# Optimization experiments

Measured on AMD Instinct MI355X. Metric: run time of the kernel, lower is better.

The kernel has to match this reference:

```python
import jax, jax.numpy as jnp
import numpy as np


def setup_inputs() -> dict:
    key = jax.random.key(0)
    ks = jax.random.split(key, 16)
    B, S, D = 2, 2048, 1024
    H, SH, RH = 16, 1, 3
    hd = D // H
    w = 1.0 / np.sqrt(D)
    return {
        "x": jax.random.normal(ks[0], (B, S, D), jnp.float32),
        "Wq": jax.random.normal(ks[1], (D, D), jnp.float32) * w,
        "bq": jnp.zeros((D,), jnp.float32),
        "Wk": jax.random.normal(ks[2], (D, D), jnp.float32) * w,
        "bk": jnp.zeros((D,), jnp.float32),
        "Wv": jax.random.normal(ks[3], (D, D), jnp.float32) * w,
        "bv": jnp.zeros((D,), jnp.float32),
        "Wproj": jax.random.normal(ks[4], (D, D), jnp.float32) * w,
        "bproj": jnp.zeros((D,), jnp.float32),
        "Wr": jax.random.normal(ks[5], (D, H - SH), jnp.float32) * w,
        "br": jnp.zeros((H - SH,), jnp.float32),
        "Ws": jax.random.normal(ks[6], (D, 2), jnp.float32) * w,
        "bs": jnp.zeros((2,), jnp.float32),
        "temperature": jnp.zeros((H, 1, 1), jnp.float32),
        "query_embedding": jax.random.truncated_normal(ks[7], -2.0, 2.0, (H, 1, hd), jnp.float32) * 0.02,
        "num_heads": H,
        "shared_heads": SH,
        "routed_heads": RH,
    }


def reference(x, Wq, bq, Wk, bk, Wv, bv, Wproj, bproj, Wr, br, Ws, bs,
              temperature, query_embedding, num_heads, shared_heads, routed_heads):
    B, S, D = x.shape
    H = num_heads
    hd = D // H

    def split_heads(t):  # [B,S,D] -> [B,H,S,hd]
        return t.reshape(B, S, H, hd).transpose(0, 2, 1, 3)

    q = split_heads(x @ Wq + bq)
    k = split_heads(x @ Wk + bk)
    v = split_heads(x @ Wv + bv)

    # L2-normalize q along head_dim, add learned query embedding, scale by softplus(temperature)
    q_norm = q * jax.lax.rsqrt(jnp.sum(q * q, axis=-1, keepdims=True) + 1e-12)
    q_scaled = (q_norm + query_embedding[None]) * jax.nn.softplus(temperature)[None]

    attn = jnp.einsum('bhqd,bhkd->bhqk', q_scaled, k) / jnp.sqrt(jnp.float32(hd))
    attn = jax.nn.softmax(attn, axis=-1)
    o = jnp.einsum('bhqk,bhkd->bhqd', attn, v)
    o = o.transpose(0, 2, 1, 3).reshape(B, S, D)  # [B,S,D]

    # Routed-head gating via top-k router
    gates = jax.nn.softmax(o @ Wr + br, axis=-1)          # [B,S,H-SH]
    _, idx = jax.lax.top_k(gates, routed_heads)           # [B,S,RH]
    mask = jax.nn.one_hot(idx, H - shared_heads, dtype=gates.dtype).sum(axis=2)
    routed_gates = gates * mask * jnp.float32(routed_heads)

    # Shared-head gating
    sw = jax.nn.softmax(o @ Ws + bs, axis=-1)             # [B,S,2]
    shared_gates = sw * jnp.float32(shared_heads)
    w0 = sw * 2.0
    shared_gates = w0[..., 0:1] * shared_gates
    routed_gates = w0[..., 1:2] * routed_gates
    masked_gates = jnp.concatenate([shared_gates, routed_gates], axis=-1)

    # einsum('bnh,bnd->bnd') sums over h: scales o by sum of gates
    o = masked_gates.sum(axis=-1, keepdims=True) * o
    return o @ Wproj + bproj
```

## Files before the change

kernel.cpp:

```cpp
#include <hip/hip_runtime.h>
#include <hip/hip_bf16.h>

typedef unsigned short ushort_t;
typedef unsigned int uint_t;

typedef __attribute__((ext_vector_type(8))) short bf8;
typedef __attribute__((ext_vector_type(4))) float f4;
typedef __attribute__((ext_vector_type(16))) float f16v;

__device__ __forceinline__ float bf2f(ushort_t u) {
    unsigned int x = ((unsigned int)u) << 16;
    return __uint_as_float(x);
}
__device__ __forceinline__ ushort_t f2bf(float f) {
    unsigned int x = __float_as_uint(f);
    unsigned int r = x + 0x7fffu + ((x >> 16) & 1u);
    return (ushort_t)(r >> 16);
}
__device__ __forceinline__ uint_t pack2bf(float a, float b) {
    return (uint_t)f2bf(a) | ((uint_t)f2bf(b) << 16);
}

__device__ __forceinline__ void gl2lds16(const ushort_t* g, ushort_t* l) {
    __builtin_amdgcn_global_load_lds(
        (const __attribute__((address_space(1))) void*)g,
        (__attribute__((address_space(3))) void*)l, 16, 0, 0);
}

__global__ __launch_bounds__(256)
void prep(const float* __restrict__ src, ushort_t* __restrict__ dst,
          const float* __restrict__ Wr, const float* __restrict__ Ws,
          ushort_t* __restrict__ Wg)
{
    int bid = blockIdx.x;
    if (bid < 4096) {
        int i = bid * 256 + threadIdx.x;
        float4 v = ((const float4*)src)[i];
        uint2 o;
        o.x = pack2bf(v.x, v.y);
        o.y = pack2bf(v.z, v.w);
        ((uint2*)dst)[i] = o;
    } else {
        int idx = (bid - 4096) * 256 + threadIdx.x;
        int c = idx >> 10, d = idx & 1023;
        float v = 0.f;
        if (c < 15) v = Wr[(size_t)d * 15 + c];
        else if (c < 17) v = Ws[(size_t)d * 2 + (c - 15)];
        Wg[idx] = f2bf(v);
    }
}

__global__ __launch_bounds__(256)
void wtrans(const float* __restrict__ W0, const float* __restrict__ W1,
            const float* __restrict__ W2, const float* __restrict__ W3,
            ushort_t* __restrict__ T0, ushort_t* __restrict__ T1,
            ushort_t* __restrict__ T2, ushort_t* __restrict__ T3)
{
    __shared__ float tile[32][33];
    const float* W; ushort_t* T;
    switch (blockIdx.z) {
        case 0: W = W0; T = T0; break;
        case 1: W = W1; T = T1; break;
        case 2: W = W2; T = T2; break;
        default: W = W3; T = T3; break;
    }
    int k0 = blockIdx.x * 32, n0 = blockIdx.y * 32;
    int t = threadIdx.x;
    int r = t >> 3, c4 = (t & 7) * 4;
    float4 v = *(const float4*)&W[(size_t)(k0 + r) * 1024 + n0 + c4];
    tile[r][c4 + 0] = v.x; tile[r][c4 + 1] = v.y;
    tile[r][c4 + 2] = v.z; tile[r][c4 + 3] = v.w;
    __syncthreads();
    int n = t >> 3, kk = (t & 7) * 4;
    uint2 o;
    o.x = pack2bf(tile[kk][n], tile[kk + 1][n]);
    o.y = pack2bf(tile[kk + 2][n], tile[kk + 3][n]);
    *(uint2*)&T[(size_t)(n0 + n) * 1024 + k0 + kk] = o;
}

__global__ __launch_bounds__(256)
void gemmQKV(const ushort_t* __restrict__ A, const ushort_t* __restrict__ Wt3,
             const float* __restrict__ bq, const float* __restrict__ bk,
             const float* __restrict__ bv,
             ushort_t* __restrict__ Qb, ushort_t* __restrict__ Kw,
             ushort_t* __restrict__ VTw,
             const float* __restrict__ temp, const float* __restrict__ emb)
{
    const int K = 1024;
    __shared__ ushort_t As[128 * 32];
    __shared__ ushort_t Bs[128 * 32];

    int t = threadIdx.x;
    int m0 = blockIdx.x * 128;
    int y = blockIdx.y;
    int region = y >> 3;
    int n0 = (y & 7) * 128;

    int lane = t & 63, w = t >> 6;
    int lm = lane & 15, quad = lane >> 4;
    int wm = (w >> 1) * 64, wn = (w & 1) * 64;

    f4 acc[4][4] = {};

    const ushort_t* pA = &A[(size_t)(m0 + (t >> 2)) * K + (t & 3) * 8];
    const ushort_t* pB = &Wt3[(size_t)(y * 128 + (t >> 2)) * K + (t & 3) * 8];
    ushort_t* lA = &As[t * 8];
    ushort_t* lB = &Bs[t * 8];
    const size_t rstep = (size_t)64 * K;

    for (int k0 = 0; k0 < K; k0 += 32) {
        gl2lds16(pA, lA);
        gl2lds16(pA + rstep, lA + 2048);
        gl2lds16(pB, lB);
        gl2lds16(pB + rstep, lB + 2048);
        pA += 32; pB += 32;
        __syncthreads();

        bf8 af[4], bfr[4];
        #pragma unroll
        for (int mi = 0; mi < 4; mi++)
            af[mi] = *(bf8*)&As[(wm + mi * 16 + lm) * 32 + quad * 8];
        #pragma unroll
        for (int ni = 0; ni < 4; ni++)
            bfr[ni] = *(bf8*)&Bs[(wn + ni * 16 + lm) * 32 + quad * 8];
        if (region == 2) {
            #pragma unroll
            for (int mi = 0; mi < 4; mi++)
            #pragma unroll
            for (int ni = 0; ni < 4; ni++)
                acc[mi][ni] = __builtin_amdgcn_mfma_f32_16x16x32_bf16(af[mi], bfr[ni], acc[mi][ni], 0, 0, 0);
        } else {
            #pragma unroll
            for (int ni = 0; ni < 4; ni++)
            #pragma unroll
            for (int mi = 0; mi < 4; mi++)
                acc[ni][mi] = __builtin_amdgcn_mfma_f32_16x16x32_bf16(bfr[ni], af[mi], acc[ni][mi], 0, 0, 0);
        }
        __syncthreads();
    }

    if (region == 0) {
        int head = (n0 + wn) >> 6;
        float sp = log1pf(__expf(temp[head]));
        f4 bv4[4], ev4[4];
        #pragma unroll
        for (int ni = 0; ni < 4; ni++) {
            bv4[ni] = *(const f4*)&bq[n0 + wn + ni * 16 + quad * 4];
            ev4[ni] = *(const f4*)&emb[head * 64 + ni * 16 + quad * 4];
        }
        #pragma unroll
        for (int mi = 0; mi < 4; mi++) {
            float v[4][4];
            float ss = 0.f;
            #pragma unroll
            for (int ni = 0; ni < 4; ni++)
            #pragma unroll
            for (int i = 0; i < 4; i++) {
                v[ni][i] = acc[ni][mi][i] + bv4[ni][i];
                ss += v[ni][i] * v[ni][i];
            }
            ss += __shfl_xor(ss, 16, 64);
            ss += __shfl_xor(ss, 32, 64);
            float rs = rsqrtf(ss + 1e-12f);
            int tok = m0 + wm + mi * 16 + lm;
            int b = tok >> 11, s = tok & 2047;
            size_t rowb = (((size_t)(b * 16 + head)) * 2048 + s) * 64;
            #pragma unroll
            for (int ni = 0; ni < 4; ni++) {
                uint2 o;
                o.x = pack2bf((v[ni][0] * rs + ev4[ni][0]) * sp * 0.125f,
                              (v[ni][1] * rs + ev4[ni][1]) * sp * 0.125f);
                o.y = pack2bf((v[ni][2] * rs + ev4[ni][2]) * sp * 0.125f,
                              (v[ni][3] * rs + ev4[ni][3]) * sp * 0.125f);
                *(uint2*)&Qb[rowb + ni * 16 + quad * 4] = o;
            }
        }
    } else if (region == 1) {
        int head = (n0 + wn) >> 6;
        f4 bv4[4];
        #pragma unroll
        for (int ni = 0; ni < 4; ni++)
            bv4[ni] = *(const f4*)&bk[n0 + wn + ni * 16 + quad * 4];
        #pragma unroll
        for (int mi = 0; mi < 4; mi++) {
            int tok = m0 + wm + mi * 16 + lm;
            int b = tok >> 11, s = tok & 2047;
            size_t rowb = (((size_t)(b * 16 + head)) * 2048 + s) * 64;
            #pragma unroll
            for (int ni = 0; ni < 4; ni++) {
                uint2 o;
                o.x = pack2bf(acc[ni][mi][0] + bv4[ni][0], acc[ni][mi][1] + bv4[ni][1]);
                o.y = pack2bf(acc[ni][mi][2] + bv4[ni][2], acc[ni][mi][3] + bv4[ni][3]);
                *(uint2*)&Kw[rowb + ni * 16 + quad * 4] = o;
            }
        }
    } else {
        float bvv[4];
        #pragma unroll
        for (int ni = 0; ni < 4; ni++) bvv[ni] = bv[n0 + wn + ni * 16 + lm];
        #pragma unroll
        for (int mi = 0; mi < 4; mi++) {
            int gr0 = m0 + wm + mi * 16 + quad * 4;
            int b = gr0 >> 11, s0 = gr0 & 2047;
            #pragma unroll
            for (int ni = 0; ni < 4; ni++) {
                int gc = n0 + wn + ni * 16 + lm;
                int h = gc >> 6, d = gc & 63;
                uint2 o;
                o.x = pack2bf(acc[mi][ni][0] + bvv[ni], acc[mi][ni][1] + bvv[ni]);
                o.y = pack2bf(acc[mi][ni][2] + bvv[ni], acc[mi][ni][3] + bvv[ni]);
                *(uint2*)&VTw[(((size_t)(b * 16 + h)) * 64 + d) * 2048 + s0] = o;
            }
        }
    }
}

__global__ __launch_bounds__(256)
void gemmP(const ushort_t* __restrict__ A, const ushort_t* __restrict__ Wt,
           const float* __restrict__ bias, const float* __restrict__ G,
           float* __restrict__ out, int M, int N, int K)
{
    __shared__ ushort_t As[128 * 32];
    __shared__ ushort_t Bs[128 * 32];

    int t = threadIdx.x;
    int m0 = blockIdx.x * 128, n0 = blockIdx.y * 128;
    int lane = t & 63, w = t >> 6;
    int lm = lane & 15, quad = lane >> 4;
    int wm = (w >> 1) * 64, wn = (w & 1) * 64;

    f4 acc[4][4] = {};

    const ushort_t* pA = &A[(size_t)(m0 + (t >> 2)) * K + (t & 3) * 8];
    const ushort_t* pB = &Wt[(size_t)(n0 + (t >> 2)) * K + (t & 3) * 8];
    ushort_t* lA = &As[t * 8];
    ushort_t* lB = &Bs[t * 8];
    const size_t rstep = (size_t)64 * K;

    for (int k0 = 0; k0 < K; k0 += 32) {
        gl2lds16(pA, lA);
        gl2lds16(pA + rstep, lA + 2048);
        gl2lds16(pB, lB);
        gl2lds16(pB + rstep, lB + 2048);
        pA += 32; pB += 32;
        __syncthreads();

        bf8 af[4], bfr[4];
        #pragma unroll
        for (int mi = 0; mi < 4; mi++)
            af[mi] = *(bf8*)&As[(wm + mi * 16 + lm) * 32 + quad * 8];
        #pragma unroll
        for (int ni = 0; ni < 4; ni++)
            bfr[ni] = *(bf8*)&Bs[(wn + ni * 16 + lm) * 32 + quad * 8];
        #pragma unroll
        for (int ni = 0; ni < 4; ni++)
        #pragma unroll
        for (int mi = 0; mi < 4; mi++)
            acc[ni][mi] = __builtin_amdgcn_mfma_f32_16x16x32_bf16(bfr[ni], af[mi], acc[ni][mi], 0, 0, 0);
        __syncthreads();
    }

    f4 bv4[4];
    #pragma unroll
    for (int ni = 0; ni < 4; ni++)
        bv4[ni] = *(const f4*)&bias[n0 + wn + ni * 16 + quad * 4];
    #pragma unroll
    for (int mi = 0; mi < 4; mi++) {
        int tok = m0 + wm + mi * 16 + lm;
        float g = G[tok];
        size_t rowb = (size_t)tok * N + n0 + wn;
        #pragma unroll
        for (int ni = 0; ni < 4; ni++) {
            f4 o;
            #pragma unroll
            for (int i = 0; i < 4; i++) o[i] = g * acc[ni][mi][i] + bv4[ni][i];
            *(f4*)&out[rowb + ni * 16 + quad * 4] = o;
        }
    }
}

__global__ __launch_bounds__(256)
void attn(const ushort_t* __restrict__ Q, const ushort_t* __restrict__ K,
          const ushort_t* __restrict__ VT, ushort_t* __restrict__ O)
{
    __shared__ ushort_t Ks[64 * 72];
    __shared__ ushort_t Vt[64 * 72];
    __shared__ ushort_t Ps[4][32 * 72];

    int t = threadIdx.x, lane = t & 63, w = t >> 6;
    int l31 = lane & 31, hi = lane >> 5;
    int bid = blockIdx.x;
    int bh = bid & 31, qt = bid >> 5;
    size_t base = (size_t)bh * 2048 * 64;

    int tok = qt * 128 + w * 32 + l31;
    const ushort_t* qp = &Q[base + (size_t)tok * 64 + hi * 8];
    bf8 qa[4];
    #pragma unroll
    for (int c = 0; c < 4; c++) qa[c] = *(const bf8*)(qp + c * 16);

    float l_part = 0.f;
    f16v o_acc[2] = {};

    int sr = t >> 3, sc = (t & 7) * 8;
    const ushort_t* kg0 = &K[base + (size_t)sr * 64 + sc];
    const ushort_t* vg0 = &VT[base + (size_t)sr * 2048 + sc];

    for (int kb = 0; kb < 2048; kb += 64) {
        __syncthreads();
        {
            uint4 k0 = *(const uint4*)(kg0 + (size_t)kb * 64);
            uint4 k1 = *(const uint4*)(kg0 + (size_t)(kb + 32) * 64);
            uint4 v0 = *(const uint4*)(vg0 + kb);
            uint4 v1 = *(const uint4*)(vg0 + 32 * 2048 + kb);
            *(uint4*)&Ks[sr * 72 + sc] = k0;
            *(uint4*)&Ks[(sr + 32) * 72 + sc] = k1;
            *(uint4*)&Vt[sr * 72 + sc] = v0;
            *(uint4*)&Vt[(sr + 32) * 72 + sc] = v1;
        }
        __syncthreads();

        ushort_t* pw = &Ps[w][0];
        #pragma unroll
        for (int kt2 = 0; kt2 < 2; kt2++) {
            f16v s = {};
            #pragma unroll
            for (int c = 0; c < 4; c++) {
                bf8 kf = *(bf8*)&Ks[(kt2 * 32 + l31) * 72 + c * 16 + hi * 8];
                s = __builtin_amdgcn_mfma_f32_32x32x16_bf16(kf, qa[c], s, 0, 0, 0);
            }
            #pragma unroll
            for (int g = 0; g < 4; g++) {
                float p0 = __expf(s[g * 4 + 0]);
                float p1 = __expf(s[g * 4 + 1]);
                float p2 = __expf(s[g * 4 + 2]);
                float p3 = __expf(s[g * 4 + 3]);
                l_part += (p0 + p1) + (p2 + p3);
                int k0i = kt2 * 32 + g * 8 + hi * 4;
                *(uint_t*)&pw[l31 * 72 + k0i]     = pack2bf(p0, p1);
                *(uint_t*)&pw[l31 * 72 + k0i + 2] = pack2bf(p2, p3);
            }
        }

        #pragma unroll
        for (int c = 0; c < 4; c++) {
            bf8 pf = *(bf8*)&pw[l31 * 72 + c * 16 + hi * 8];
            #pragma unroll
            for (int dt = 0; dt < 2; dt++) {
                bf8 vf = *(bf8*)&Vt[(dt * 32 + l31) * 72 + c * 16 + hi * 8];
                o_acc[dt] = __builtin_amdgcn_mfma_f32_32x32x16_bf16(vf, pf, o_acc[dt], 0, 0, 0);
            }
        }
    }

    l_part += __shfl_xor(l_part, 32, 64);
    float rl = 1.f / l_part;

    int b = bh >> 4, h = bh & 15;
    size_t rowb = ((size_t)(b * 2048 + tok)) * 1024 + h * 64;
    #pragma unroll
    for (int dt = 0; dt < 2; dt++)
    #pragma unroll
    for (int g = 0; g < 4; g++) {
        int d0 = dt * 32 + g * 8 + hi * 4;
        uint2 o;
        o.x = pack2bf(o_acc[dt][g * 4 + 0] * rl, o_acc[dt][g * 4 + 1] * rl);
        o.y = pack2bf(o_acc[dt][g * 4 + 2] * rl, o_acc[dt][g * 4 + 3] * rl);
        *(uint2*)&O[rowb + d0] = o;
    }
}

__global__ __launch_bounds__(256)
void router(const ushort_t* __restrict__ O, const ushort_t* __restrict__ Wg,
            const float* __restrict__ br, const float* __restrict__ bs,
            float* __restrict__ G)
{
    __shared__ float Ls[64][21];
    int t = threadIdx.x, lane = t & 63, w = t >> 6;
    int lm = lane & 15, quad = lane >> 4;
    int tok0 = blockIdx.x * 64;

    const ushort_t* ap = &O[(size_t)(tok0 + w * 16 + lm) * 1024 + quad * 8];
    const ushort_t* b0p = &Wg[(size_t)lm * 1024 + quad * 8];
    const ushort_t* b1p = &Wg[(size_t)(16 + lm) * 1024 + quad * 8];

    f4 acc0 = {}, acc1 = {};
    for (int k0 = 0; k0 < 1024; k0 += 32) {
        bf8 a = *(const bf8*)(ap + k0);
        bf8 b0 = *(const bf8*)(b0p + k0);
        bf8 b1 = *(const bf8*)(b1p + k0);
        acc0 = __builtin_amdgcn_mfma_f32_16x16x32_bf16(a, b0, acc0, 0, 0, 0);
        acc1 = __builtin_amdgcn_mfma_f32_16x16x32_bf16(a, b1, acc1, 0, 0, 0);
    }
    #pragma unroll
    for (int i = 0; i < 4; i++) {
        int tl = w * 16 + quad * 4 + i;
        Ls[tl][lm] = acc0[i];
        if (lm == 0) Ls[tl][16] = acc1[i];
    }
    __syncthreads();
    if (t < 64) {
        float v[15];
        float mx = -1e30f;
        #pragma unroll
        for (int c = 0; c < 15; c++) { v[c] = Ls[t][c] + br[c]; mx = fmaxf(mx, v[c]); }
        float sum = 0.f;
        #pragma unroll
        for (int c = 0; c < 15; c++) { v[c] = __expf(v[c] - mx); sum += v[c]; }
        float inv = 1.f / sum;
        float t3 = 0.f;
        for (int r = 0; r < 3; r++) {
            int bi = 0; float bv = -1e30f;
            #pragma unroll
            for (int c = 0; c < 15; c++) if (v[c] > bv) { bv = v[c]; bi = c; }
            t3 += bv; v[bi] = -1e30f;
        }
        t3 *= inv;
        float a0 = Ls[t][15] + bs[0], a1 = Ls[t][16] + bs[1];
        float m2 = fmaxf(a0, a1);
        float e0 = __expf(a0 - m2), e1 = __expf(a1 - m2);
        G[tok0 + t] = (2.f * e0 + 6.f * e1 * t3) / (e0 + e1);
    }
}

extern "C" void kernel_launch(void* const* d_in, const int* in_sizes, int n_in,
                              void* d_out, int out_size, void* d_ws, size_t ws_size,
                              hipStream_t stream)
{
    const float* x     = (const float*)d_in[0];
    const float* Wq    = (const float*)d_in[1];
    const float* bq    = (const float*)d_in[2];
    const float* Wk    = (const float*)d_in[3];
    const float* bk    = (const float*)d_in[4];
    const float* Wv    = (const float*)d_in[5];
    const float* bv    = (const float*)d_in[6];
    const float* Wproj = (const float*)d_in[7];
    const float* bproj = (const float*)d_in[8];
    const float* Wr    = (const float*)d_in[9];
    const float* br    = (const float*)d_in[10];
    const float* Ws    = (const float*)d_in[11];
    const float* bs    = (const float*)d_in[12];
    const float* temp  = (const float*)d_in[13];
    const float* emb   = (const float*)d_in[14];

    const int M = 4096, N = 1024, Kd = 1024;

    char* ws = (char*)d_ws;
    ushort_t* Kw  = (ushort_t*)ws;
    ushort_t* VTw = (ushort_t*)(ws + 8388608);
    ushort_t* Qb  = (ushort_t*)(ws + 16777216);
    ushort_t* Ob  = (ushort_t*)(ws + 25165824);
    ushort_t* xb  = (ushort_t*)(ws + 33554432);
    ushort_t* Wt3 = (ushort_t*)(ws + 41943040);
    ushort_t* Wtp = (ushort_t*)(ws + 48234496);
    float*    Gw  = (float*)(ws + 50331648);
    ushort_t* Wg  = (ushort_t*)(ws + 50348032);

    prep<<<4224, 256, 0, stream>>>(x, xb, Wr, Ws, Wg);
    wtrans<<<dim3(32, 32, 4), 256, 0, stream>>>(Wq, Wk, Wv, Wproj,
        Wt3, Wt3 + 1048576, Wt3 + 2097152, Wtp);

    gemmQKV<<<dim3(32, 24), 256, 0, stream>>>(xb, Wt3, bq, bk, bv,
        Qb, Kw, VTw, temp, emb);

    attn<<<512, 256, 0, stream>>>(Qb, Kw, VTw, Ob);

    router<<<64, 256, 0, stream>>>(Ob, Wg, br, bs, Gw);

    gemmP<<<dim3(32, 8), 256, 0, stream>>>(Ob, Wtp, bproj, Gw, (float*)d_out, M, N, Kd);
}
```

Before: 263.7 us.

## Split attention over two key halves with a combine kernel; merge prep launches

Attention now splits the key range into two halves, doubling the grid from 512 to 1024 blocks. Each half writes unnormalized partial outputs and row sums, and a new combine kernel sums them, normalizes, and writes the head-interleaved output. The weight transpose is folded into the prep kernel to save a launch, and a cheaper round-to-bf16 pack replaces the exact rounding in attention. This is meant to raise occupancy on a GPU with many CUs, at the cost of an extra kernel, more traffic through partial buffers, and buffers that alias one another in the workspace.

After: 265.2 us. About the same (+0.6%).

```diff
diff --git a/kernel.cpp b/kernel.cpp
--- a/kernel.cpp
+++ b/kernel.cpp
@@ -20,6 +20,11 @@
 __device__ __forceinline__ uint_t pack2bf(float a, float b) {
     return (uint_t)f2bf(a) | ((uint_t)f2bf(b) << 16);
 }
+__device__ __forceinline__ uint_t pack2bf_fast(float a, float b) {
+    uint_t au = __float_as_uint(a) + 0x8000u;
+    uint_t bu = __float_as_uint(b) + 0x8000u;
+    return __builtin_amdgcn_perm(bu, au, 0x07060302);
+}
 
 __device__ __forceinline__ void gl2lds16(const ushort_t* g, ushort_t* l) {
     __builtin_amdgcn_global_load_lds(
@@ -28,54 +33,53 @@
 }
 
 __global__ __launch_bounds__(256)
-void prep(const float* __restrict__ src, ushort_t* __restrict__ dst,
+void prep(const float* __restrict__ x, ushort_t* __restrict__ xb,
           const float* __restrict__ Wr, const float* __restrict__ Ws,
-          ushort_t* __restrict__ Wg)
-{
+          ushort_t* __restrict__ Wg,
+          const float* __restrict__ W0, const float* __restrict__ W1,
+          const float* __restrict__ W2, const float* __restrict__ W3,
+          ushort_t* __restrict__ T0, ushort_t* __restrict__ T1,
+          ushort_t* __restrict__ T2, ushort_t* __restrict__ T3)
+{
+    __shared__ float tile[32][33];
     int bid = blockIdx.x;
+    int t = threadIdx.x;
     if (bid < 4096) {
-        int i = bid * 256 + threadIdx.x;
-        float4 v = ((const float4*)src)[i];
+        int i = bid * 256 + t;
+        float4 v = ((const float4*)x)[i];
         uint2 o;
         o.x = pack2bf(v.x, v.y);
         o.y = pack2bf(v.z, v.w);
-        ((uint2*)dst)[i] = o;
-    } else {
-        int idx = (bid - 4096) * 256 + threadIdx.x;
+        ((uint2*)xb)[i] = o;
+    } else if (bid < 4224) {
+        int idx = (bid - 4096) * 256 + t;
         int c = idx >> 10, d = idx & 1023;
         float v = 0.f;
         if (c < 15) v = Wr[(size_t)d * 15 + c];
         else if (c < 17) v = Ws[(size_t)d * 2 + (c - 15)];
         Wg[idx] = f2bf(v);
-    }
-}
-
-__global__ __launch_bounds__(256)
-void wtrans(const float* __restrict__ W0, const float* __restrict__ W1,
-            const float* __restrict__ W2, const float* __restrict__ W3,
-            ushort_t* __restrict__ T0, ushort_t* __restrict__ T1,
-            ushort_t* __restrict__ T2, ushort_t* __restrict__ T3)
-{
-    __shared__ float tile[32][33];
-    const float* W; ushort_t* T;
-    switch (blockIdx.z) {
-        case 0: W = W0; T = T0; break;
-        case 1: W = W1; T = T1; break;
-        case 2: W = W2; T = T2; break;
-        default: W = W3; T = T3; break;
-    }
-    int k0 = blockIdx.x * 32, n0 = blockIdx.y * 32;
-    int t = threadIdx.x;
-    int r = t >> 3, c4 = (t & 7) * 4;
-    float4 v = *(const float4*)&W[(size_t)(k0 + r) * 1024 + n0 + c4];
-    tile[r][c4 + 0] = v.x; tile[r][c4 + 1] = v.y;
-    tile[r][c4 + 2] = v.z; tile[r][c4 + 3] = v.w;
-    __syncthreads();
-    int n = t >> 3, kk = (t & 7) * 4;
-    uint2 o;
-    o.x = pack2bf(tile[kk][n], tile[kk + 1][n]);
-    o.y = pack2bf(tile[kk + 2][n], tile[kk + 3][n]);
-    *(uint2*)&T[(size_t)(n0 + n) * 1024 + k0 + kk] = o;
+    } else {
+        int idx = bid - 4224;
+        int z = idx >> 10, r10 = idx & 1023;
+        int k0 = (r10 & 31) * 32, n0 = (r10 >> 5) * 32;
+        const float* W; ushort_t* T;
+        switch (z) {
+            case 0: W = W0; T = T0; break;
+            case 1: W = W1; T = T1; break;
+            case 2: W = W2; T = T2; break;
+            default: W = W3; T = T3; break;
+        }
+        int r = t >> 3, c4 = (t & 7) * 4;
+        float4 v = *(const float4*)&W[(size_t)(k0 + r) * 1024 + n0 + c4];
+        tile[r][c4 + 0] = v.x; tile[r][c4 + 1] = v.y;
+        tile[r][c4 + 2] = v.z; tile[r][c4 + 3] = v.w;
+        __syncthreads();
+        int n = t >> 3, kk = (t & 7) * 4;
+        uint2 o;
+        o.x = pack2bf(tile[kk][n], tile[kk + 1][n]);
+        o.y = pack2bf(tile[kk + 2][n], tile[kk + 3][n]);
+        *(uint2*)&T[(size_t)(n0 + n) * 1024 + k0 + kk] = o;
+    }
 }
 
 __global__ __launch_bounds__(256)
@@ -281,7 +285,8 @@
 
 __global__ __launch_bounds__(256)
 void attn(const ushort_t* __restrict__ Q, const ushort_t* __restrict__ K,
-          const ushort_t* __restrict__ VT, ushort_t* __restrict__ O)
+          const ushort_t* __restrict__ VT, ushort_t* __restrict__ Opart,
+          float* __restrict__ Lw)
 {
     __shared__ ushort_t Ks[64 * 72];
     __shared__ ushort_t Vt[64 * 72];
@@ -290,7 +295,7 @@
     int t = threadIdx.x, lane = t & 63, w = t >> 6;
     int l31 = lane & 31, hi = lane >> 5;
     int bid = blockIdx.x;
-    int bh = bid & 31, qt = bid >> 5;
+    int bh = bid & 31, qt = (bid >> 5) & 15, ks = bid >> 9;
     size_t base = (size_t)bh * 2048 * 64;
 
     int tok = qt * 128 + w * 32 + l31;
@@ -306,7 +311,8 @@
     const ushort_t* kg0 = &K[base + (size_t)sr * 64 + sc];
     const ushort_t* vg0 = &VT[base + (size_t)sr * 2048 + sc];
 
-    for (int kb = 0; kb < 2048; kb += 64) {
+    int kend = ks * 1024 + 1024;
+    for (int kb = ks * 1024; kb < kend; kb += 64) {
         __syncthreads();
         {
             uint4 k0 = *(const uint4*)(kg0 + (size_t)kb * 64);
@@ -337,8 +343,8 @@
                 float p3 = __expf(s[g * 4 + 3]);
                 l_part += (p0 + p1) + (p2 + p3);
                 int k0i = kt2 * 32 + g * 8 + hi * 4;
-                *(uint_t*)&pw[l31 * 72 + k0i]     = pack2bf(p0, p1);
-                *(uint_t*)&pw[l31 * 72 + k0i + 2] = pack2bf(p2, p3);
+                *(uint_t*)&pw[l31 * 72 + k0i]     = pack2bf_fast(p0, p1);
+                *(uint_t*)&pw[l31 * 72 + k0i + 2] = pack2bf_fast(p2, p3);
             }
         }
 
@@ -354,20 +360,42 @@
     }
 
     l_part += __shfl_xor(l_part, 32, 64);
-    float rl = 1.f / l_part;
-
-    int b = bh >> 4, h = bh & 15;
-    size_t rowb = ((size_t)(b * 2048 + tok)) * 1024 + h * 64;
+    if (hi == 0) Lw[((size_t)ks * 32 + bh) * 2048 + tok] = l_part;
+
+    size_t pbase = (((size_t)(ks * 32 + bh)) * 2048 + tok) * 64;
     #pragma unroll
     for (int dt = 0; dt < 2; dt++)
     #pragma unroll
     for (int g = 0; g < 4; g++) {
         int d0 = dt * 32 + g * 8 + hi * 4;
         uint2 o;
-        o.x = pack2bf(o_acc[dt][g * 4 + 0] * rl, o_acc[dt][g * 4 + 1] * rl);
-        o.y = pack2bf(o_acc[dt][g * 4 + 2] * rl, o_acc[dt][g * 4 + 3] * rl);
-        *(uint2*)&O[rowb + d0] = o;
-    }
+        o.x = pack2bf_fast(o_acc[dt][g * 4 + 0], o_acc[dt][g * 4 + 1]);
+        o.y = pack2bf_fast(o_acc[dt][g * 4 + 2], o_acc[dt][g * 4 + 3]);
+        *(uint2*)&Opart[pbase + d0] = o;
+    }
+}
+
+__global__ __launch_bounds__(256)
+void combine(const ushort_t* __restrict__ Opart, const float* __restrict__ Lw,
+             ushort_t* __restrict__ Ob)
+{
+    int i = blockIdx.x * 256 + threadIdx.x;
+    int flat = i * 4;
+    int row = flat >> 6;
+    int d = flat & 63;
+    int bh = row >> 11, tok = row & 2047;
+    int b = bh >> 4, h = bh & 15;
+    float rl = 1.f / (Lw[row] + Lw[65536 + row]);
+    uint2 p0 = *(const uint2*)&Opart[flat];
+    uint2 p1 = *(const uint2*)&Opart[4194304 + flat];
+    float v0 = (bf2f(p0.x & 0xffff) + bf2f(p1.x & 0xffff)) * rl;
+    float v1 = (bf2f(p0.x >> 16)   + bf2f(p1.x >> 16))   * rl;
+    float v2 = (bf2f(p0.y & 0xffff) + bf2f(p1.y & 0xffff)) * rl;
+    float v3 = (bf2f(p0.y >> 16)   + bf2f(p1.y >> 16))   * rl;
+    uint2 o;
+    o.x = pack2bf(v0, v1);
+    o.y = pack2bf(v2, v3);
+    *(uint2*)&Ob[((size_t)(b * 2048 + tok)) * 1024 + h * 64 + d] = o;
 }
 
 __global__ __launch_bounds__(256)
@@ -446,24 +474,27 @@
     const int M = 4096, N = 1024, Kd = 1024;
 
     char* ws = (char*)d_ws;
-    ushort_t* Kw  = (ushort_t*)ws;
-    ushort_t* VTw = (ushort_t*)(ws + 8388608);
-    ushort_t* Qb  = (ushort_t*)(ws + 16777216);
-    ushort_t* Ob  = (ushort_t*)(ws + 25165824);
-    ushort_t* xb  = (ushort_t*)(ws + 33554432);
-    ushort_t* Wt3 = (ushort_t*)(ws + 41943040);
-    ushort_t* Wtp = (ushort_t*)(ws + 48234496);
-    float*    Gw  = (float*)(ws + 50331648);
-    ushort_t* Wg  = (ushort_t*)(ws + 50348032);
-
-    prep<<<4224, 256, 0, stream>>>(x, xb, Wr, Ws, Wg);
-    wtrans<<<dim3(32, 32, 4), 256, 0, stream>>>(Wq, Wk, Wv, Wproj,
+    ushort_t* Kw    = (ushort_t*)ws;
+    ushort_t* VTw   = (ushort_t*)(ws + 8388608);
+    ushort_t* Qb    = (ushort_t*)(ws + 16777216);
+    ushort_t* Wtp   = (ushort_t*)(ws + 25165824);
+    float*    Gw    = (float*)(ws + 27262976);
+    ushort_t* Wg    = (ushort_t*)(ws + 27279360);
+    float*    Lw    = (float*)(ws + 27344896);
+    ushort_t* Wt3   = (ushort_t*)(ws + 27869184);
+    ushort_t* xb    = (ushort_t*)(ws + 34160640);
+    ushort_t* Opart = (ushort_t*)(ws + 27869184);
+    ushort_t* Ob    = Qb;
+
+    prep<<<8320, 256, 0, stream>>>(x, xb, Wr, Ws, Wg, Wq, Wk, Wv, Wproj,
         Wt3, Wt3 + 1048576, Wt3 + 2097152, Wtp);
 
     gemmQKV<<<dim3(32, 24), 256, 0, stream>>>(xb, Wt3, bq, bk, bv,
         Qb, Kw, VTw, temp, emb);
 
-    attn<<<512, 256, 0, stream>>>(Qb, Kw, VTw, Ob);
+    attn<<<1024, 256, 0, stream>>>(Qb, Kw, VTw, Opart, Lw);
+
+    combine<<<4096, 256, 0, stream>>>(Opart, Lw, Ob);
 
     router<<<64, 256, 0, stream>>>(Ob, Wg, br, bs, Gw);
 
```
